# Optimization experiments

Measured on AMD Instinct MI355X. Metric: run time of the kernel, lower is better.

Reference implementation:

```python
import jax, jax.numpy as jnp
import numpy as np

B, N, K = 8, 16384, 32
EPS = 1e-5


def setup_inputs() -> dict:
    key = jax.random.key(0)
    ks = jax.random.split(key, 11)
    xyz = jax.random.normal(ks[0], (B, N, 3), jnp.float32)
    intensity = jax.random.normal(ks[1], (B, 3, N), jnp.float32)
    indices = jax.random.randint(ks[2], (B, N, K), 0, N)
    # linear_p: Conv2d(3,3,1)+BN+ReLU, then Conv2d(3,1,1)
    w1 = jax.random.normal(ks[3], (3, 3), jnp.float32) * 0.3
    b1 = jax.random.normal(ks[4], (3,), jnp.float32) * 0.1
    gamma = jax.random.uniform(ks[5], (3,), jnp.float32, 0.5, 1.5)
    beta = jax.random.normal(ks[6], (3,), jnp.float32) * 0.1
    mean = jax.random.normal(ks[7], (3,), jnp.float32) * 0.1
    var = jax.random.uniform(ks[8], (3,), jnp.float32, 0.5, 1.5)
    w2 = jax.random.normal(ks[9], (1, 3), jnp.float32) * 0.3
    b2 = jax.random.normal(ks[10], (1,), jnp.float32) * 0.1
    return dict(xyz=xyz, intensity=intensity, indices=indices, w1=w1, b1=b1,
                gamma=gamma, beta=beta, mean=mean, var=var, w2=w2, b2=b2)


def reference(xyz, intensity, indices, w1, b1, gamma, beta, mean, var, w2, b2):
    # neighbor gathers (irregular access)
    xyz_nb = jax.vmap(lambda p, i: p[i])(xyz, indices)          # [B,N,K,3]
    i_nb = jax.vmap(lambda ft, i: ft[:, i])(intensity, indices)  # [B,3,N,K]
    # relative position + gaussian kernel
    pos = xyz_nb - xyz[:, :, None, :]                            # [B,N,K,3]
    pos_g = jnp.exp(-2.0 * pos * pos)
    pos_g = jnp.transpose(pos_g, (0, 3, 1, 2))                   # [B,3,N,K]
    # 1x1 conv (3->3) + eval-mode BN + ReLU
    h = jnp.einsum('oc,bcnk->bonk', w1, pos_g) + b1[None, :, None, None]
    scale = gamma / jnp.sqrt(var + EPS)
    h = (h - mean[None, :, None, None]) * scale[None, :, None, None] + beta[None, :, None, None]
    h = jax.nn.relu(h)
    # 1x1 conv (3->1), softmax over neighbors
    w = jnp.einsum('oc,bcnk->bonk', w2, h) + b2[None, :, None, None]  # [B,1,N,K]
    w = jax.nn.softmax(w, axis=-1)
    # weighted reduce over neighbors
    return jnp.sum(i_nb * w, axis=-1)                            # [B,3,N]
```

## Files before the change

kernel.cpp:

```cpp
#include <hip/hip_runtime.h>
#include <math.h>

#define PB 8
#define PN 16384
#define PK 32
#define PEPS 1e-5f

__global__ __launch_bounds__(256) void sa_pack(
    const float* __restrict__ xyz,
    const float* __restrict__ intensity,
    float4* __restrict__ packed)
{
    const int t = blockIdx.x * 256 + threadIdx.x;
    const int b = t >> 14;
    const int n = t & (PN - 1);
    const float x = xyz[(long)t * 3 + 0];
    const float y = xyz[(long)t * 3 + 1];
    const float z = xyz[(long)t * 3 + 2];
    const float* ib = intensity + (long)b * 3 * PN;
    const float i0 = ib[0 * PN + n];
    const float i1 = ib[1 * PN + n];
    const float i2 = ib[2 * PN + n];
    packed[(long)t * 2 + 0] = make_float4(x, y, z, 0.f);
    packed[(long)t * 2 + 1] = make_float4(i0, i1, i2, 0.f);
}

__global__ __launch_bounds__(256) void sa_main(
    const float4* __restrict__ packed,
    const int*   __restrict__ indices,
    const float* __restrict__ w1, const float* __restrict__ b1,
    const float* __restrict__ gamma_, const float* __restrict__ beta_,
    const float* __restrict__ mean_, const float* __restrict__ var_,
    const float* __restrict__ w2, const float* __restrict__ b2,
    float* __restrict__ out)
{
    const int lane = threadIdx.x & 31;
    const int grp  = threadIdx.x >> 5;
    const long ng  = (long)blockIdx.x * 8 + grp;
    const int b = (int)(ng >> 14);
    const int n = (int)(ng & (PN - 1));

    float A[3][3], d[3], wv[3];
#pragma unroll
    for (int o = 0; o < 3; ++o) {
        const float sc = gamma_[o] * rsqrtf(var_[o] + PEPS);
#pragma unroll
        for (int c = 0; c < 3; ++c) A[o][c] = w1[o * 3 + c] * sc;
        d[o]  = (b1[o] - mean_[o]) * sc + beta_[o];
        wv[o] = w2[o];
    }
    const float bias2 = b2[0];

    const long bn = (long)b * PN + n;

    const float4 c0 = packed[bn * 2];

    const int idx = indices[bn * PK + lane];
    const long bi = ((long)b * PN + idx) * 2;

    const float4 v0 = packed[bi + 0];
    const float4 v1 = packed[bi + 1];

    const float px = v0.x - c0.x;
    const float py = v0.y - c0.y;
    const float pz = v0.z - c0.z;

    const float g0 = __expf(-2.f * px * px);
    const float g1 = __expf(-2.f * py * py);
    const float g2 = __expf(-2.f * pz * pz);

    float logit = bias2;
#pragma unroll
    for (int o = 0; o < 3; ++o) {
        float h = A[o][0] * g0 + A[o][1] * g1 + A[o][2] * g2 + d[o];
        h = fmaxf(h, 0.f);
        logit = fmaf(wv[o], h, logit);
    }

    float m = logit;
#pragma unroll
    for (int s = 16; s > 0; s >>= 1) m = fmaxf(m, __shfl_xor(m, s, 64));

    const float e = __expf(logit - m);

    float ssum = e;
    float a0 = e * v1.x;
    float a1 = e * v1.y;
    float a2 = e * v1.z;
#pragma unroll
    for (int s = 16; s > 0; s >>= 1) {
        ssum += __shfl_xor(ssum, s, 64);
        a0   += __shfl_xor(a0, s, 64);
        a1   += __shfl_xor(a1, s, 64);
        a2   += __shfl_xor(a2, s, 64);
    }

    if (lane == 0) {
        const float inv = 1.f / ssum;
        float* ob = out + (long)b * 3 * PN;
        ob[0 * PN + n] = a0 * inv;
        ob[1 * PN + n] = a1 * inv;
        ob[2 * PN + n] = a2 * inv;
    }
}

__global__ __launch_bounds__(256) void sa_fallback(
    const float* __restrict__ xyz, const float* __restrict__ intensity,
    const int* __restrict__ indices,
    const float* __restrict__ w1, const float* __restrict__ b1,
    const float* __restrict__ gamma_, const float* __restrict__ beta_,
    const float* __restrict__ mean_, const float* __restrict__ var_,
    const float* __restrict__ w2, const float* __restrict__ b2,
    float* __restrict__ out)
{
    const int lane = threadIdx.x & 31;
    const int grp  = threadIdx.x >> 5;
    const long ng  = (long)blockIdx.x * 8 + grp;
    const int b = (int)(ng >> 14);
    const int n = (int)(ng & (PN - 1));

    float A[3][3], d[3], wv[3];
#pragma unroll
    for (int o = 0; o < 3; ++o) {
        const float sc = gamma_[o] * rsqrtf(var_[o] + PEPS);
#pragma unroll
        for (int c = 0; c < 3; ++c) A[o][c] = w1[o * 3 + c] * sc;
        d[o]  = (b1[o] - mean_[o]) * sc + beta_[o];
        wv[o] = w2[o];
    }
    const float bias2 = b2[0];
    const long bn = (long)b * PN + n;
    const float cx = xyz[bn * 3 + 0], cy = xyz[bn * 3 + 1], cz = xyz[bn * 3 + 2];
    const int idx = indices[bn * PK + lane];
    const long bi = (long)b * PN + idx;
    const float px = xyz[bi * 3 + 0] - cx;
    const float py = xyz[bi * 3 + 1] - cy;
    const float pz = xyz[bi * 3 + 2] - cz;
    const float g0 = __expf(-2.f * px * px);
    const float g1 = __expf(-2.f * py * py);
    const float g2 = __expf(-2.f * pz * pz);
    float logit = bias2;
#pragma unroll
    for (int o = 0; o < 3; ++o) {
        float h = A[o][0] * g0 + A[o][1] * g1 + A[o][2] * g2 + d[o];
        h = fmaxf(h, 0.f);
        logit = fmaf(wv[o], h, logit);
    }
    float m = logit;
#pragma unroll
    for (int s = 16; s > 0; s >>= 1) m = fmaxf(m, __shfl_xor(m, s, 64));
    const float e = __expf(logit - m);
    const float* ib = intensity + (long)b * 3 * PN;
    float ssum = e;
    float a0 = e * ib[0 * PN + idx];
    float a1 = e * ib[1 * PN + idx];
    float a2 = e * ib[2 * PN + idx];
#pragma unroll
    for (int s = 16; s > 0; s >>= 1) {
        ssum += __shfl_xor(ssum, s, 64);
        a0 += __shfl_xor(a0, s, 64);
        a1 += __shfl_xor(a1, s, 64);
        a2 += __shfl_xor(a2, s, 64);
    }
    if (lane == 0) {
        const float inv = 1.f / ssum;
        float* ob = out + (long)b * 3 * PN;
        ob[0 * PN + n] = a0 * inv;
        ob[1 * PN + n] = a1 * inv;
        ob[2 * PN + n] = a2 * inv;
    }
}

extern "C" void kernel_launch(void* const* d_in, const int* in_sizes, int n_in,
                              void* d_out, int out_size, void* d_ws, size_t ws_size,
                              hipStream_t stream) {
    const float* xyz       = (const float*)d_in[0];
    const float* intensity = (const float*)d_in[1];
    const int*   indices   = (const int*)d_in[2];
    const float* w1        = (const float*)d_in[3];
    const float* b1        = (const float*)d_in[4];
    const float* gamma_    = (const float*)d_in[5];
    const float* beta_     = (const float*)d_in[6];
    const float* mean_     = (const float*)d_in[7];
    const float* var_      = (const float*)d_in[8];
    const float* w2        = (const float*)d_in[9];
    const float* b2        = (const float*)d_in[10];
    float* out = (float*)d_out;

    const int points = PB * PN;
    const size_t packed_bytes = (size_t)points * 32;

    if (ws_size >= packed_bytes) {
        float4* packed = (float4*)d_ws;
        sa_pack<<<points / 256, 256, 0, stream>>>(xyz, intensity, packed);
        sa_main<<<points / 8, 256, 0, stream>>>(packed, indices, w1, b1, gamma_,
                                                beta_, mean_, var_, w2, b2, out);
    } else {
        sa_fallback<<<points / 8, 256, 0, stream>>>(xyz, intensity, indices, w1, b1,
                                                    gamma_, beta_, mean_, var_, w2, b2, out);
    }
}
```

Before: 121.7 us.

## Pack point records as fp16, drop softmax max, use DPP reductions

The packed per-point record (xyz + intensity) is stored as eight halves in 16 bytes instead of two float4s, halving the gather traffic for neighbor lookups. Folded BN/conv constants are precomputed once into the workspace by the pack kernel instead of per thread. The softmax max-subtraction is removed, relying on bounded logits, and the cross-lane sums use DPP row operations ending in lane 31 instead of xor shuffles. This trades accuracy (fp16 coordinates and intensities) and overflow safety for fewer bytes and instructions.

```diff
diff --git a/kernel.cpp b/kernel.cpp
--- a/kernel.cpp
+++ b/kernel.cpp
@@ -1,4 +1,5 @@
 #include <hip/hip_runtime.h>
+#include <hip/hip_fp16.h>
 #include <math.h>
 
 #define PB 8
@@ -6,10 +7,29 @@
 #define PK 32
 #define PEPS 1e-5f
 
+template <int CTRL>
+__device__ __forceinline__ float dpp_add_step(float v) {
+    int t = __builtin_amdgcn_update_dpp(0, __float_as_int(v), CTRL, 0xf, 0xf, true);
+    return v + __int_as_float(t);
+}
+__device__ __forceinline__ float reduce32_to_lane31(float v) {
+    v = dpp_add_step<0x111>(v);
+    v = dpp_add_step<0x112>(v);
+    v = dpp_add_step<0x114>(v);
+    v = dpp_add_step<0x118>(v);
+    v = dpp_add_step<0x142>(v);
+    return v;
+}
+
 __global__ __launch_bounds__(256) void sa_pack(
     const float* __restrict__ xyz,
     const float* __restrict__ intensity,
-    float4* __restrict__ packed)
+    uint4* __restrict__ packed,
+    const float* __restrict__ w1, const float* __restrict__ b1,
+    const float* __restrict__ gamma_, const float* __restrict__ beta_,
+    const float* __restrict__ mean_, const float* __restrict__ var_,
+    const float* __restrict__ w2, const float* __restrict__ b2,
+    float* __restrict__ cst)
 {
     const int t = blockIdx.x * 256 + threadIdx.x;
     const int b = t >> 14;
@@ -21,82 +41,80 @@
     const float i0 = ib[0 * PN + n];
     const float i1 = ib[1 * PN + n];
     const float i2 = ib[2 * PN + n];
-    packed[(long)t * 2 + 0] = make_float4(x, y, z, 0.f);
-    packed[(long)t * 2 + 1] = make_float4(i0, i1, i2, 0.f);
+
+    union { __half2 h2[4]; uint4 u; } rec;
+    const __half hz = __float2half_rn(z);
+    rec.h2[0] = __halves2half2(__float2half_rn(x), __float2half_rn(y));
+    rec.h2[1] = __halves2half2(hz, __float2half_rn(0.f));
+    rec.h2[2] = __halves2half2(__float2half_rn(i0), __float2half_rn(i1));
+    rec.h2[3] = __halves2half2(__float2half_rn(i2), __float2half_rn(0.f));
+    packed[t] = rec.u;
+
+    if (t == 0) {
+        for (int o = 0; o < 3; ++o) {
+            const float sc = gamma_[o] * rsqrtf(var_[o] + PEPS);
+            for (int c = 0; c < 3; ++c) cst[o * 3 + c] = w1[o * 3 + c] * sc;
+            cst[9 + o]  = (b1[o] - mean_[o]) * sc + beta_[o];
+            cst[12 + o] = w2[o];
+        }
+        cst[15] = b2[0];
+    }
 }
 
 __global__ __launch_bounds__(256) void sa_main(
-    const float4* __restrict__ packed,
+    const uint4* __restrict__ packed,
     const int*   __restrict__ indices,
-    const float* __restrict__ w1, const float* __restrict__ b1,
-    const float* __restrict__ gamma_, const float* __restrict__ beta_,
-    const float* __restrict__ mean_, const float* __restrict__ var_,
-    const float* __restrict__ w2, const float* __restrict__ b2,
+    const float* __restrict__ cst,
     float* __restrict__ out)
 {
     const int lane = threadIdx.x & 31;
     const int grp  = threadIdx.x >> 5;
-    const long ng  = (long)blockIdx.x * 8 + grp;
-    const int b = (int)(ng >> 14);
-    const int n = (int)(ng & (PN - 1));
-
-    float A[3][3], d[3], wv[3];
-#pragma unroll
-    for (int o = 0; o < 3; ++o) {
-        const float sc = gamma_[o] * rsqrtf(var_[o] + PEPS);
-#pragma unroll
-        for (int c = 0; c < 3; ++c) A[o][c] = w1[o * 3 + c] * sc;
-        d[o]  = (b1[o] - mean_[o]) * sc + beta_[o];
-        wv[o] = w2[o];
-    }
-    const float bias2 = b2[0];
-
-    const long bn = (long)b * PN + n;
-
-    const float4 c0 = packed[bn * 2];
-
-    const int idx = indices[bn * PK + lane];
-    const long bi = ((long)b * PN + idx) * 2;
-
-    const float4 v0 = packed[bi + 0];
-    const float4 v1 = packed[bi + 1];
-
-    const float px = v0.x - c0.x;
-    const float py = v0.y - c0.y;
-    const float pz = v0.z - c0.z;
+    const int ng   = blockIdx.x * 8 + grp;
+    const int b = ng >> 14;
+    const int n = ng & (PN - 1);
+
+    const float A00 = cst[0], A01 = cst[1], A02 = cst[2];
+    const float A10 = cst[3], A11 = cst[4], A12 = cst[5];
+    const float A20 = cst[6], A21 = cst[7], A22 = cst[8];
+    const float d0 = cst[9], d1 = cst[10], d2 = cst[11];
+    const float w0 = cst[12], w1v = cst[13], w2v = cst[14];
+    const float bias2 = cst[15];
+
+    const uint4 c = packed[ng];
+    const float2 cxy = __half22float2(*(const __half2*)&c.x);
+    const float  cz  = __half2float(*(const __half*)&c.y);
+
+    const int idx = indices[(long)ng * PK + lane];
+    const uint4 r = packed[(b << 14) | idx];
+
+    const float2 nxy = __half22float2(*(const __half2*)&r.x);
+    const float  nz  = __half2float(*(const __half*)&r.y);
+    const float2 ni01 = __half22float2(*(const __half2*)&r.z);
+    const float  ni2  = __half2float(*(const __half*)&r.w);
+
+    const float px = nxy.x - cxy.x;
+    const float py = nxy.y - cxy.y;
+    const float pz = nz - cz;
 
     const float g0 = __expf(-2.f * px * px);
     const float g1 = __expf(-2.f * py * py);
     const float g2 = __expf(-2.f * pz * pz);
 
-    float logit = bias2;
-#pragma unroll
-    for (int o = 0; o < 3; ++o) {
-        float h = A[o][0] * g0 + A[o][1] * g1 + A[o][2] * g2 + d[o];
-        h = fmaxf(h, 0.f);
-        logit = fmaf(wv[o], h, logit);
-    }
-
-    float m = logit;
-#pragma unroll
-    for (int s = 16; s > 0; s >>= 1) m = fmaxf(m, __shfl_xor(m, s, 64));
-
-    const float e = __expf(logit - m);
-
-    float ssum = e;
-    float a0 = e * v1.x;
-    float a1 = e * v1.y;
-    float a2 = e * v1.z;
-#pragma unroll
-    for (int s = 16; s > 0; s >>= 1) {
-        ssum += __shfl_xor(ssum, s, 64);
-        a0   += __shfl_xor(a0, s, 64);
-        a1   += __shfl_xor(a1, s, 64);
-        a2   += __shfl_xor(a2, s, 64);
-    }
-
-    if (lane == 0) {
-        const float inv = 1.f / ssum;
+    float h0 = fmaf(A00, g0, fmaf(A01, g1, fmaf(A02, g2, d0)));
+    float h1 = fmaf(A10, g0, fmaf(A11, g1, fmaf(A12, g2, d1)));
+    float h2 = fmaf(A20, g0, fmaf(A21, g1, fmaf(A22, g2, d2)));
+    h0 = fmaxf(h0, 0.f); h1 = fmaxf(h1, 0.f); h2 = fmaxf(h2, 0.f);
+    const float logit = fmaf(w0, h0, fmaf(w1v, h1, fmaf(w2v, h2, bias2)));
+
+    const float e = __expf(logit);
+
+    float s  = reduce32_to_lane31(e);
+    float a0 = reduce32_to_lane31(e * ni01.x);
+    float a1 = reduce32_to_lane31(e * ni01.y);
+    float a2 = reduce32_to_lane31(e * ni2);
+
+    if (lane == 31) {
+        const float inv = 1.f / s;
         float* ob = out + (long)b * 3 * PN;
         ob[0 * PN + n] = a0 * inv;
         ob[1 * PN + n] = a1 * inv;
@@ -188,13 +206,16 @@
     float* out = (float*)d_out;
 
     const int points = PB * PN;
-    const size_t packed_bytes = (size_t)points * 32;
-
-    if (ws_size >= packed_bytes) {
-        float4* packed = (float4*)d_ws;
-        sa_pack<<<points / 256, 256, 0, stream>>>(xyz, intensity, packed);
-        sa_main<<<points / 8, 256, 0, stream>>>(packed, indices, w1, b1, gamma_,
-                                                beta_, mean_, var_, w2, b2, out);
+    const size_t rec_bytes = (size_t)points * 16;
+    const size_t need = rec_bytes + 64;
+
+    if (ws_size >= need) {
+        uint4* packed = (uint4*)d_ws;
+        float* cst = (float*)((char*)d_ws + rec_bytes);
+        sa_pack<<<points / 256, 256, 0, stream>>>(xyz, intensity, packed,
+                                                  w1, b1, gamma_, beta_, mean_,
+                                                  var_, w2, b2, cst);
+        sa_main<<<points / 8, 256, 0, stream>>>(packed, indices, cst, out);
     } else {
         sa_fallback<<<points / 8, 256, 0, stream>>>(xyz, intensity, indices, w1, b1,
                                                     gamma_, beta_, mean_, var_, w2, b2, out);
```

After: 115.5 us. 5.1% less time.
